# Kernel optimization log

Hardware: AMD Instinct MI355X
Metric: run time of the kernel (lower is better)

## Reference

```python
import jax, jax.numpy as jnp
import numpy as np

L = 4        # num_layers
N = 50000    # nodes
E = 500000   # edges
B = 32       # graphs
H = 64       # hidden_dim
HP = 16      # hidden_dim_pe
P = 8        # pe_dim
BN_EPS = 1e-5


def setup_inputs() -> dict:
    key = jax.random.key(0)
    ks = jax.random.split(key, 22)
    nrm = lambda k, s: jax.random.normal(k, s, dtype=jnp.float32)
    w = lambda k, s: nrm(k, s) * 0.1
    return {
        'x': nrm(ks[0], (N, H)),
        'pe': nrm(ks[1], (N, P)),
        'Lambda': jax.random.uniform(ks[2], (B, P), dtype=jnp.float32),
        'edge_attr': nrm(ks[3], (E, H)),
        'edge_index': jax.random.randint(ks[4], (2, E), 0, N),
        'batch': jnp.sort(jax.random.randint(ks[5], (N,), 0, B)),
        # edge encoder (SPE): eigenvalue MLP + output projection
        'We1': w(ks[6], (L, P, HP * P)), 'be1': jnp.zeros((L, HP * P)),
        'Wee': w(ks[7], (L, HP, H)),     'bee': jnp.zeros((L, H)),
        # GINE mlp: Linear-BN-ReLU-Linear
        'W1': w(ks[8], (L, H, H)), 'b1': jnp.zeros((L, H)),
        'g1': jnp.ones((L, H)),    'beta1': jnp.zeros((L, H)),
        'W2': w(ks[9], (L, H, H)), 'b2': jnp.zeros((L, H)),
        # equivariant PE conv: edge gate + channel Linear
        'Wg': w(ks[10], (L, H, HP)),  'bg': jnp.zeros((L, HP)),
        'Wp': w(ks[11], (L, HP, HP)), 'bp': jnp.zeros((L, HP)),
        # outer BatchNorm per layer
        'gn': jnp.ones((L, H)), 'bnb': jnp.zeros((L, H)),
    }


def _bn(h, gamma, beta):
    mu = h.mean(0)
    var = h.var(0)
    return gamma * (h - mu) * jax.lax.rsqrt(var + BN_EPS) + beta


def reference(x, pe, Lambda, edge_attr, We1, be1, Wee, bee, W1, b1, g1, beta1,
              W2, b2, Wg, bg, Wp, bp, gn, bnb, edge_index, batch):
    src, dst = edge_index[0], edge_index[1]
    bsrc = batch[src]                       # [E] graph id of source node
    z = jnp.tile(pe[:, None, :], (1, HP, 1))  # [N, HP, P]
    for i in range(L):
        # SPE edge encoder: phi(Lambda)-weighted inner product over pe axis
        phi = jax.nn.relu(Lambda @ We1[i] + be1[i]).reshape(B, HP, P)
        eh = jnp.einsum('ehp,ehp->eh', phi[bsrc] * z[src], z[dst])  # [E, HP]
        ea = eh @ Wee[i] + bee[i] + edge_attr                       # [E, H]
        # GINEConv: scatter-add of relu(x_src + edge_attr), eps = 0
        agg = jax.ops.segment_sum(jax.nn.relu(x[src] + ea), dst, num_segments=N)
        h = x + agg
        h = jax.nn.relu(_bn(h @ W1[i] + b1[i], g1[i], beta1[i])) @ W2[i] + b2[i]
        # GINConvEquivariant: gated scatter-add, Linear on channel axis
        gate = jax.nn.relu(ea @ Wg[i] + bg[i])                      # [E, HP]
        msgz = jax.nn.relu(z[src] + gate[:, :, None])               # [E, HP, P]
        z = z + jax.ops.segment_sum(msgz, dst, num_segments=N)
        z = jnp.einsum('nhp,hk->nkp', z, Wp[i]) + bp[i][None, :, None]
        x = _bn(h, gn[i], bnb[i])
        if i != L - 1:
            x = jax.nn.relu(x)
    return x, z
```

## Files before the change

kernel.cpp:

```cpp
#include <hip/hip_runtime.h>

#define NN 50000
#define EE 500000
#define LL 4

typedef unsigned short u16;
typedef unsigned int u32;

__device__ __forceinline__ float bfc(u16 u) { return __uint_as_float(((u32)u) << 16); }
__device__ __forceinline__ u16 f2bf(float f) {
    u32 u = __float_as_uint(f);
    return (u16)((u + 0x7fffu + ((u >> 16) & 1u)) >> 16);
}
__device__ __forceinline__ float lanebc(float v, int l) {
    return __int_as_float(__builtin_amdgcn_readlane(__float_as_int(v), l));
}
__device__ __forceinline__ void unpack2(u32 w, float& lo, float& hi) {
    lo = __uint_as_float(w << 16);
    hi = __uint_as_float(w & 0xffff0000u);
}

__global__ __launch_bounds__(256) void k_init(const float* __restrict__ x, float* __restrict__ Xf,
                                              u16* __restrict__ Xh, int big,
                                              int* __restrict__ deg, int* __restrict__ cursor) {
    for (int i = blockIdx.x * 256 + threadIdx.x; i < NN * 64; i += gridDim.x * 256) {
        if (big) Xh[i] = f2bf(x[i]);
        else Xf[i] = x[i];
    }
    for (int i = blockIdx.x * 256 + threadIdx.x; i < NN; i += gridDim.x * 256) {
        deg[i] = 0;
        cursor[i] = 0;
    }
}

__global__ __launch_bounds__(128) void k_phi(const float* __restrict__ Lam, const float* __restrict__ We1,
                                             const float* __restrict__ be1, float* __restrict__ phiA) {
    int l = blockIdx.x >> 5, b = blockIdx.x & 31, j = threadIdx.x;
    float acc = be1[l * 128 + j];
    for (int q = 0; q < 8; q++)
        acc = fmaf(Lam[b * 8 + q], We1[l * 1024 + q * 128 + j], acc);
    phiA[l * 4096 + b * 128 + j] = fmaxf(acc, 0.f);
}

__global__ __launch_bounds__(256) void k_small(const float* __restrict__ Wee, const float* __restrict__ Wg,
                                               float* __restrict__ MA) {
    int l = blockIdx.x, t = threadIdx.x;
    int k = t >> 4, h = t & 15;
    float m = 0.f;
    for (int f = 0; f < 64; f++)
        m = fmaf(Wee[l * 1024 + k * 64 + f], Wg[l * 1024 + f * 16 + h], m);
    MA[l * 256 + t] = m;
}

__global__ __launch_bounds__(256) void k_hist(const int* __restrict__ ei, int* __restrict__ deg) {
    int e = blockIdx.x * 256 + threadIdx.x;
    if (e < EE) {
        int d = ei[EE + e];
        if (d >= 0 && d < NN) atomicAdd(&deg[d], 1);
    }
}

__global__ __launch_bounds__(256) void k_scan1(const int* __restrict__ deg, int* __restrict__ rowptr,
                                               int* __restrict__ bsum) {
    __shared__ int tmp[256];
    int t = threadIdx.x, i = blockIdx.x * 256 + t;
    int v = (i < NN) ? deg[i] : 0;
    tmp[t] = v;
    __syncthreads();
    for (int off = 1; off < 256; off <<= 1) {
        int a = (t >= off) ? tmp[t - off] : 0;
        __syncthreads();
        tmp[t] += a;
        __syncthreads();
    }
    if (i < NN) rowptr[i] = tmp[t] - v;
    if (t == 255) bsum[blockIdx.x] = tmp[255];
}

__global__ __launch_bounds__(256) void k_scan2(const int* __restrict__ bsum, int* __restrict__ boff,
                                               int* __restrict__ rowptr, int nb) {
    __shared__ int tmp[256];
    int t = threadIdx.x;
    int v = (t < nb) ? bsum[t] : 0;
    tmp[t] = v;
    __syncthreads();
    for (int off = 1; off < 256; off <<= 1) {
        int a = (t >= off) ? tmp[t - off] : 0;
        __syncthreads();
        tmp[t] += a;
        __syncthreads();
    }
    if (t < nb) boff[t] = tmp[t] - v;
    if (t == 255) rowptr[NN] = tmp[255];
}

__global__ __launch_bounds__(256) void k_scan3(int* __restrict__ rowptr, const int* __restrict__ boff) {
    int i = blockIdx.x * 256 + threadIdx.x;
    if (i < NN) rowptr[i] += boff[blockIdx.x];
}

__global__ __launch_bounds__(256) void k_scatter(const int* __restrict__ ei, const int* __restrict__ batch,
                                                 const int* __restrict__ rowptr, int* __restrict__ cursor,
                                                 u32* __restrict__ sb, int* __restrict__ eeo) {
    int e = blockIdx.x * 256 + threadIdx.x;
    if (e < EE) {
        int s = ei[e], d = ei[EE + e];
        if (s < 0) s = 0; if (s >= NN) s = NN - 1;
        if (d < 0) d = 0; if (d >= NN) d = NN - 1;
        int pos = rowptr[d] + atomicAdd(&cursor[d], 1);
        if (pos >= 0 && pos < EE) {
            sb[pos] = (u32)s | ((u32)(batch[s] & 31) << 16);
            eeo[pos] = e;
        }
    }
}

__global__ __launch_bounds__(256) void k_perm(const float* __restrict__ eat, const int* __restrict__ eeo,
                                              u16* __restrict__ eatp) {
    const float4* e4 = reinterpret_cast<const float4*>(eat);
    ushort4* o4 = reinterpret_cast<ushort4*>(eatp);
    for (long long i = (long long)blockIdx.x * 256 + threadIdx.x; i < (long long)EE * 16;
         i += (long long)gridDim.x * 256) {
        int idx = (int)(i >> 4), cc = (int)(i & 15);
        int e = eeo[idx];
        float4 v = e4[(size_t)e * 16 + cc];
        ushort4 o;
        o.x = f2bf(v.x); o.y = f2bf(v.y); o.z = f2bf(v.z); o.w = f2bf(v.w);
        o4[i] = o;
    }
}

__global__ __launch_bounds__(256) void k_eag_all(const u16* __restrict__ eatp, const float* __restrict__ Wg,
                                                 const float* __restrict__ bee, const float* __restrict__ bg,
                                                 u32* __restrict__ EAGp4) {
    __shared__ float sWg[4096];
    __shared__ float scv[64];
    __shared__ u32 srow[256][33];
    const int t = threadIdx.x;
    for (int i = t; i < 4096; i += 256) sWg[i] = Wg[i];
    __syncthreads();
    if (t < 64) {
        const int l = t >> 4, h = t & 15;
        float c = bg[l * 16 + h];
        for (int j = 0; j < 64; j++) c = fmaf(bee[l * 64 + j], sWg[l * 1024 + j * 16 + h], c);
        scv[t] = c;
    }
    const int base = blockIdx.x * 256;
    const u32* eat32 = (const u32*)eatp;
    for (int i = t; i < 256 * 32; i += 256) {
        int r = i >> 5, c = i & 31;
        int idx = base + r;
        srow[r][c] = (idx < EE) ? eat32[(size_t)idx * 32 + c] : 0u;
    }
    __syncthreads();
    const int idx = base + t;
    if (idx >= EE) return;
#pragma unroll
    for (int l = 0; l < LL; l++) {
        const float* wl = &sWg[l * 1024];
        float acc[16];
#pragma unroll
        for (int h = 0; h < 16; h++) acc[h] = scv[l * 16 + h];
#pragma unroll
        for (int c = 0; c < 32; c++) {
            float a0, a1;
            unpack2(srow[t][c], a0, a1);
            const float* w0 = &wl[(2 * c) * 16];
#pragma unroll
            for (int h = 0; h < 16; h++) acc[h] = fmaf(a0, w0[h], fmaf(a1, w0[16 + h], acc[h]));
        }
        u32 w[8];
#pragma unroll
        for (int h = 0; h < 8; h++) w[h] = (u32)f2bf(acc[h]) | ((u32)f2bf(acc[8 + h]) << 16);
        uint4* op = reinterpret_cast<uint4*>(EAGp4 + (size_t)l * EE * 8 + (size_t)idx * 8);
        op[0] = make_uint4(w[0], w[1], w[2], w[3]);
        op[1] = make_uint4(w[4], w[5], w[6], w[7]);
    }
}

__global__ __launch_bounds__(256) void k_eag2(const u16* __restrict__ eatp, const float* __restrict__ WgL,
                                              const float* __restrict__ beeL, const float* __restrict__ bgL,
                                              u32* __restrict__ EAGp) {
    __shared__ float sWg[1024];
    __shared__ float scv[16];
    __shared__ u32 srow[256][33];
    const int t = threadIdx.x;
    for (int i = t; i < 1024; i += 256) sWg[i] = WgL[i];
    __syncthreads();
    if (t < 16) {
        float c = bgL[t];
        for (int j = 0; j < 64; j++) c = fmaf(beeL[j], sWg[j * 16 + t], c);
        scv[t] = c;
    }
    const int base = blockIdx.x * 256;
    const u32* eat32 = (const u32*)eatp;
    for (int i = t; i < 256 * 32; i += 256) {
        int r = i >> 5, c = i & 31;
        int idx = base + r;
        srow[r][c] = (idx < EE) ? eat32[(size_t)idx * 32 + c] : 0u;
    }
    __syncthreads();
    const int idx = base + t;
    if (idx < EE) {
        float acc[16];
#pragma unroll
        for (int h = 0; h < 16; h++) acc[h] = scv[h];
#pragma unroll
        for (int c = 0; c < 32; c++) {
            float a0, a1;
            unpack2(srow[t][c], a0, a1);
            const float* w0 = &sWg[(2 * c) * 16];
#pragma unroll
            for (int h = 0; h < 16; h++) acc[h] = fmaf(a0, w0[h], fmaf(a1, w0[16 + h], acc[h]));
        }
        u32 w[8];
#pragma unroll
        for (int h = 0; h < 8; h++) w[h] = (u32)f2bf(acc[h]) | ((u32)f2bf(acc[8 + h]) << 16);
        uint4* op = reinterpret_cast<uint4*>(EAGp + (size_t)idx * 8);
        op[0] = make_uint4(w[0], w[1], w[2], w[3]);
        op[1] = make_uint4(w[4], w[5], w[6], w[7]);
    }
}

#define EF(P, kk) do { \
    P##w = (u32)__builtin_amdgcn_readlane((int)svec, (kk)); \
    int s_ = (int)(P##w & 0xffffu); \
    if (INM == 0) { P##z0 = P##z1 = pe[s_ * 8 + pp]; } \
    else { float2 t_ = Z2[s_ * 64 + lane]; P##z0 = t_.x; P##z1 = t_.y; } \
    P##xs = bfc(Xh[s_ * 64 + lane]); \
    size_t ge_ = (size_t)(c + (kk)); \
    P##ea = bfc(eatp[ge_ * 64 + lane]); \
    unpack2(EAGp[ge_ * 8 + hlo], P##gl, P##gh); \
} while (0)

#define EC(P, MSK) do { \
    int b_ = (int)((P##w >> 16) & 31u); \
    float p0 = sphi[b_ * 128 + lane] * P##z0 * zd0; \
    float p1 = sphi[b_ * 128 + 64 + lane] * P##z1 * zd1; \
    p0 += __shfl_xor(p0, 1); p1 += __shfl_xor(p1, 1); \
    p0 += __shfl_xor(p0, 2); p1 += __shfl_xor(p1, 2); \
    p0 += __shfl_xor(p0, 4); p1 += __shfl_xor(p1, 4); \
    float eaA = 0.f, eaB = 0.f, gA = P##gl, gB = 0.f, hA = P##gh, hB = 0.f; \
    _Pragma("unroll") \
    for (int k_ = 0; k_ < 8; k_++) { float e_ = lanebc(p0, k_ << 3); \
        eaA = fmaf(e_, wee[k_], eaA); gA = fmaf(e_, mlo[k_], gA); hA = fmaf(e_, mhi[k_], hA); } \
    _Pragma("unroll") \
    for (int k_ = 0; k_ < 8; k_++) { float e_ = lanebc(p1, k_ << 3); \
        eaB = fmaf(e_, wee[8 + k_], eaB); gB = fmaf(e_, mlo[8 + k_], gB); hB = fmaf(e_, mhi[8 + k_], hB); } \
    float ea_ = beev + P##ea + eaA + eaB; \
    accx = fmaf(MSK, fmaxf(0.f, P##xs + ea_), accx); \
    az0  = fmaf(MSK, fmaxf(0.f, P##z0 + fmaxf(gA + gB, 0.f)), az0); \
    az1  = fmaf(MSK, fmaxf(0.f, P##z1 + fmaxf(hA + hB, 0.f)), az1); \
} while (0)

template <int INM, int FIN>
__global__ __launch_bounds__(256) void k_edge2(const float2* __restrict__ Z2,
                                               const float* __restrict__ pe,
                                               const u16* __restrict__ Xh,
                                               const u16* __restrict__ eatp, const u32* __restrict__ EAGp,
                                               const int* __restrict__ rowptr, const u32* __restrict__ sb,
                                               const float* __restrict__ phiL, const float* __restrict__ WeeL,
                                               const float* __restrict__ beeL, const float* __restrict__ ML,
                                               const float* __restrict__ WpL, const float* __restrict__ bpL,
                                               float* __restrict__ Hf, float2* __restrict__ Z2O,
                                               float* __restrict__ outz,
                                               double* __restrict__ stats) {
    __shared__ float sphi[4096];
    __shared__ float sWp[256];
    __shared__ float sbp[16];
    if (blockIdx.x == 0) stats[threadIdx.x] = 0.0;
    for (int t = threadIdx.x; t < 4096; t += 256) sphi[t] = phiL[t];
    if (threadIdx.x < 256) sWp[threadIdx.x] = WpL[threadIdx.x];
    if (threadIdx.x < 16) sbp[threadIdx.x] = bpL[threadIdx.x];
    const int lane = threadIdx.x & 63;
    const int wid = threadIdx.x >> 6;
    const int hlo = lane >> 3;
    const int pp = lane & 7;
    float wee[16], mlo[16], mhi[16];
#pragma unroll
    for (int k = 0; k < 16; k++) {
        wee[k] = WeeL[k * 64 + lane];
        mlo[k] = ML[k * 16 + hlo];
        mhi[k] = ML[k * 16 + 8 + hlo];
    }
    const float beev = beeL[lane];
    __syncthreads();
    for (int n = blockIdx.x * 4 + wid; n < NN; n += gridDim.x * 4) {
        float zd0, zd1;
        if (INM == 0) { zd0 = zd1 = pe[n * 8 + pp]; }
        else { float2 t = Z2[n * 64 + lane]; zd0 = t.x; zd1 = t.y; }
        float accx = bfc(Xh[n * 64 + lane]);
        float az0 = zd0, az1 = zd1;
        int i0 = rowptr[n], i1 = rowptr[n + 1];
        if (i0 < 0) i0 = 0;
        if (i1 > EE) i1 = EE;
        for (int c = i0; c < i1; c += 64) {
            const int ce = (c + 64 < i1) ? c + 64 : i1;
            const int m = ce - c;
            const int mL = m - 1;
            int ci = c + lane; if (ci > i1 - 1) ci = i1 - 1;
            const u32 svec = sb[ci];
            u32 Aw, Bw, Nw, Mw;
            float Az0, Az1, Axs, Aea, Agl, Agh;
            float Bz0, Bz1, Bxs, Bea, Bgl, Bgh;
            float Nz0, Nz1, Nxs, Nea, Ngl, Ngh;
            float Mz0, Mz1, Mxs, Mea, Mgl, Mgh;
            EF(A, 0);
            EF(B, (1 > mL ? mL : 1));
            for (int k = 0; k < m; k += 2) {
                const int n0 = (k + 2 > mL) ? mL : k + 2;
                const int n1 = (k + 3 > mL) ? mL : k + 3;
                EF(N, n0);
                EF(M, n1);
                EC(A, 1.f);
                EC(B, (k + 1 <= mL) ? 1.f : 0.f);
                Aw = Nw; Az0 = Nz0; Az1 = Nz1; Axs = Nxs; Aea = Nea; Agl = Ngl; Agh = Ngh;
                Bw = Mw; Bz0 = Mz0; Bz1 = Mz1; Bxs = Mxs; Bea = Mea; Bgl = Mgl; Bgh = Mgh;
            }
        }
        Hf[n * 64 + lane] = accx;
        float r0 = sbp[hlo], r1 = sbp[8 + hlo];
#pragma unroll
        for (int h = 0; h < 8; h++) {
            const float v = __shfl(az0, (h << 3) + pp);
            r0 = fmaf(v, sWp[h * 16 + hlo], r0);
            r1 = fmaf(v, sWp[h * 16 + 8 + hlo], r1);
        }
#pragma unroll
        for (int h = 0; h < 8; h++) {
            const float v = __shfl(az1, (h << 3) + pp);
            r0 = fmaf(v, sWp[(8 + h) * 16 + hlo], r0);
            r1 = fmaf(v, sWp[(8 + h) * 16 + 8 + hlo], r1);
        }
        if (FIN) {
            outz[n * 128 + lane] = r0;
            outz[n * 128 + 64 + lane] = r1;
        } else {
            Z2O[n * 64 + lane] = make_float2(r0, r1);
        }
    }
}

template <int INM>
__global__ __launch_bounds__(256) void k_edge_s(const float* __restrict__ Zf,
                                                const float* __restrict__ pe,
                                                const float* __restrict__ Xf, const float* __restrict__ eat,
                                                const int* __restrict__ rowptr, const u32* __restrict__ sb,
                                                const int* __restrict__ eeo,
                                                const float* __restrict__ phiL, const float* __restrict__ WeeL,
                                                const float* __restrict__ beeL,
                                                const float* __restrict__ WgL, const float* __restrict__ bgL,
                                                const float* __restrict__ WpL, const float* __restrict__ bpL,
                                                float* __restrict__ Hf, float* __restrict__ ZfO,
                                                double* __restrict__ stats) {
    __shared__ float sphi[32 * 128];
    __shared__ float sWp[256];
    __shared__ float sbp[16];
    if (blockIdx.x == 0) stats[threadIdx.x] = 0.0;
    for (int t = threadIdx.x; t < 4096; t += 256) sphi[t] = phiL[t];
    if (threadIdx.x < 256) sWp[threadIdx.x] = WpL[threadIdx.x];
    if (threadIdx.x < 16) sbp[threadIdx.x] = bpL[threadIdx.x];
    const int lane = threadIdx.x & 63;
    const int wid = threadIdx.x >> 6;
    const int hlo = lane >> 3;
    const int pp = lane & 7;
    const int h16 = lane & 15;
    const int g16 = lane & 48;
    float wee[16], wgr[16];
#pragma unroll
    for (int k = 0; k < 16; k++) {
        wee[k] = WeeL[k * 64 + lane];
        wgr[k] = WgL[(g16 + k) * 16 + h16];
    }
    const float beev = beeL[lane];
    const float bgr = bgL[h16];
    __syncthreads();
    for (int n = blockIdx.x * 4 + wid; n < NN; n += gridDim.x * 4) {
        float zd0, zd1;
        if (INM == 0) { zd0 = zd1 = pe[n * 8 + pp]; }
        else { zd0 = Zf[n * 128 + lane]; zd1 = Zf[n * 128 + 64 + lane]; }
        float accx = Xf[n * 64 + lane];
        float az0 = zd0, az1 = zd1;
        int i0 = rowptr[n], i1 = rowptr[n + 1];
        if (i0 < 0) i0 = 0;
        if (i1 > EE) i1 = EE;
        for (int idx = i0; idx < i1; ++idx) {
            const u32 w = sb[idx];
            const int s = w & 0xffff;
            const int b = (w >> 16) & 31;
            int e = eeo[idx];
            e = (e < 0) ? 0 : ((e >= EE) ? EE - 1 : e);
            float zs0, zs1;
            if (INM == 0) { zs0 = zs1 = pe[s * 8 + pp]; }
            else { zs0 = Zf[s * 128 + lane]; zs1 = Zf[s * 128 + 64 + lane]; }
            float p0 = sphi[b * 128 + lane] * zs0 * zd0;
            float p1 = sphi[b * 128 + 64 + lane] * zs1 * zd1;
            p0 += __shfl_xor(p0, 1); p1 += __shfl_xor(p1, 1);
            p0 += __shfl_xor(p0, 2); p1 += __shfl_xor(p1, 2);
            p0 += __shfl_xor(p0, 4); p1 += __shfl_xor(p1, 4);
            float ea = beev + eat[(size_t)e * 64 + lane];
#pragma unroll
            for (int k = 0; k < 8; k++) ea = fmaf(lanebc(p0, k << 3), wee[k], ea);
#pragma unroll
            for (int k = 0; k < 8; k++) ea = fmaf(lanebc(p1, k << 3), wee[8 + k], ea);
            float gp = 0.f;
#pragma unroll
            for (int i = 0; i < 16; i++) gp = fmaf(__shfl(ea, g16 + i), wgr[i], gp);
            gp += __shfl_xor(gp, 16);
            gp += __shfl_xor(gp, 32);
            const float gv = fmaxf(gp + bgr, 0.f);
            const float glo = __shfl(gv, hlo);
            const float ghi = __shfl(gv, 8 + hlo);
            const float xs = Xf[s * 64 + lane];
            accx += fmaxf(0.f, xs + ea);
            az0 += fmaxf(0.f, zs0 + glo);
            az1 += fmaxf(0.f, zs1 + ghi);
        }
        Hf[n * 64 + lane] = accx;
        float r0 = sbp[hlo], r1 = sbp[8 + hlo];
#pragma unroll
        for (int h = 0; h < 8; h++) {
            const float v = __shfl(az0, (h << 3) + pp);
            r0 = fmaf(v, sWp[h * 16 + hlo], r0);
            r1 = fmaf(v, sWp[h * 16 + 8 + hlo], r1);
        }
#pragma unroll
        for (int h = 0; h < 8; h++) {
            const float v = __shfl(az1, (h << 3) + pp);
            r0 = fmaf(v, sWp[(8 + h) * 16 + hlo], r0);
            r1 = fmaf(v, sWp[(8 + h) * 16 + 8 + hlo], r1);
        }
        ZfO[n * 128 + lane] = r0;
        ZfO[n * 128 + 64 + lane] = r1;
    }
}

__global__ __launch_bounds__(256) void k_gemm1(float* Buf, const float* __restrict__ WL,
                                               const float* __restrict__ bL,
                                               double* __restrict__ sum, double* __restrict__ sq) {
    __shared__ float sW[4096];
    __shared__ double red[512];
    for (int t = threadIdx.x; t < 4096; t += 256) sW[t] = WL[t];
    const int lane = threadIdx.x & 63, wid = threadIdx.x >> 6;
    const float bv = bL[lane];
    __syncthreads();
    double s = 0.0, q = 0.0;
    for (int n = blockIdx.x * 4 + wid; n < NN; n += gridDim.x * 4) {
        const float h = Buf[n * 64 + lane];
        float a0 = bv, a1 = 0.f;
#pragma unroll
        for (int k = 0; k < 32; k++) a0 = fmaf(lanebc(h, k), sW[k * 64 + lane], a0);
#pragma unroll
        for (int k = 32; k < 64; k++) a1 = fmaf(lanebc(h, k), sW[k * 64 + lane], a1);
        const float acc = a0 + a1;
        Buf[n * 64 + lane] = acc;
        s += (double)acc;
        q += (double)acc * (double)acc;
    }
    red[threadIdx.x] = s;
    red[256 + threadIdx.x] = q;
    __syncthreads();
    if (threadIdx.x < 64) {
        s = red[threadIdx.x] + red[threadIdx.x + 64] + red[threadIdx.x + 128] + red[threadIdx.x + 192];
        q = red[256 + threadIdx.x] + red[320 + threadIdx.x] + red[384 + threadIdx.x] + red[448 + threadIdx.x];
        atomicAdd(&sum[lane], s);
        atomicAdd(&sq[lane], q);
    }
}

__global__ __launch_bounds__(256) void k_gemm2(float* Buf, const float* __restrict__ WL,
                                               const float* __restrict__ bL,
                                               const float* __restrict__ gL, const float* __restrict__ betaL,
                                               const double* __restrict__ s1, const double* __restrict__ q1,
                                               double* __restrict__ sum, double* __restrict__ sq) {
    __shared__ float sW[4096];
    __shared__ double red[512];
    for (int t = threadIdx.x; t < 4096; t += 256) sW[t] = WL[t];
    const int lane = threadIdx.x & 63, wid = threadIdx.x >> 6;
    const float bv = bL[lane];
    const double mu = s1[lane] * (1.0 / NN);
    const double var = q1[lane] * (1.0 / NN) - mu * mu;
    const float inv = rsqrtf(fmaxf((float)var, 0.f) + 1e-5f);
    const float gm = gL[lane] * inv;
    const float ga = betaL[lane] - (float)mu * gm;
    __syncthreads();
    double s = 0.0, q = 0.0;
    for (int n = blockIdx.x * 4 + wid; n < NN; n += gridDim.x * 4) {
        const float v = Buf[n * 64 + lane];
        const float r = fmaxf(fmaf(v, gm, ga), 0.f);
        float a0 = bv, a1 = 0.f;
#pragma unroll
        for (int k = 0; k < 32; k++) a0 = fmaf(lanebc(r, k), sW[k * 64 + lane], a0);
#pragma unroll
        for (int k = 32; k < 64; k++) a1 = fmaf(lanebc(r, k), sW[k * 64 + lane], a1);
        const float acc = a0 + a1;
        Buf[n * 64 + lane] = acc;
        s += (double)acc;
        q += (double)acc * (double)acc;
    }
    red[threadIdx.x] = s;
    red[256 + threadIdx.x] = q;
    __syncthreads();
    if (threadIdx.x < 64) {
        s = red[threadIdx.x] + red[threadIdx.x + 64] + red[threadIdx.x + 128] + red[threadIdx.x + 192];
        q = red[256 + threadIdx.x] + red[320 + threadIdx.x] + red[384 + threadIdx.x] + red[448 + threadIdx.x];
        atomicAdd(&sum[lane], s);
        atomicAdd(&sq[lane], q);
    }
}

__global__ __launch_bounds__(256) void k_bnout2(const float* __restrict__ In, u16* __restrict__ Xh,
                                                float* __restrict__ outx,
                                                const double* __restrict__ s2, const double* __restrict__ q2,
                                                const float* __restrict__ gL, const float* __restrict__ bL,
                                                int last) {
    int i = blockIdx.x * 256 + threadIdx.x;
    const int f = i & 63;
    const double mu = s2[f] * (1.0 / NN);
    const double var = q2[f] * (1.0 / NN) - mu * mu;
    const float inv = rsqrtf(fmaxf((float)var, 0.f) + 1e-5f);
    const float gm = gL[f] * inv;
    const float ga = bL[f] - (float)mu * gm;
    for (; i < NN * 64; i += gridDim.x * 256) {
        float o = fmaf(In[i], gm, ga);
        if (last) {
            outx[i] = o;
        } else {
            o = fmaxf(o, 0.f);
            Xh[i] = f2bf(o);
        }
    }
}

__global__ __launch_bounds__(256) void k_bnout(const float* __restrict__ In, float* __restrict__ Xf,
                                               const double* __restrict__ s2, const double* __restrict__ q2,
                                               const float* __restrict__ gL, const float* __restrict__ bL,
                                               int dorelu) {
    int i = blockIdx.x * 256 + threadIdx.x;
    const int f = i & 63;
    const double mu = s2[f] * (1.0 / NN);
    const double var = q2[f] * (1.0 / NN) - mu * mu;
    const float inv = rsqrtf(fmaxf((float)var, 0.f) + 1e-5f);
    const float gm = gL[f] * inv;
    const float ga = bL[f] - (float)mu * gm;
    for (; i < NN * 64; i += gridDim.x * 256) {
        float o = fmaf(In[i], gm, ga);
        if (dorelu) o = fmaxf(o, 0.f);
        Xf[i] = o;
    }
}

extern "C" void kernel_launch(void* const* d_in, const int* in_sizes, int n_in,
                              void* d_out, int out_size, void* d_ws, size_t ws_size,
                              hipStream_t stream) {
    (void)in_sizes; (void)n_in; (void)out_size;
    const float* x    = (const float*)d_in[0];
    const float* pe   = (const float*)d_in[1];
    const float* Lam  = (const float*)d_in[2];
    const float* eat  = (const float*)d_in[3];
    const int*   ei   = (const int*)d_in[4];
    const int*   batch= (const int*)d_in[5];
    const float* We1  = (const float*)d_in[6];
    const float* be1  = (const float*)d_in[7];
    const float* Wee  = (const float*)d_in[8];
    const float* bee  = (const float*)d_in[9];
    const float* W1   = (const float*)d_in[10];
    const float* b1   = (const float*)d_in[11];
    const float* g1   = (const float*)d_in[12];
    const float* bt1  = (const float*)d_in[13];
    const float* W2   = (const float*)d_in[14];
    const float* b2   = (const float*)d_in[15];
    const float* Wg   = (const float*)d_in[16];
    const float* bg   = (const float*)d_in[17];
    const float* Wp   = (const float*)d_in[18];
    const float* bp   = (const float*)d_in[19];
    const float* gn   = (const float*)d_in[20];
    const float* bnb  = (const float*)d_in[21];

    float* Xf   = (float*)d_out;
    u16*   Xh   = (u16*)d_out;
    float* B    = (float*)d_out + 3200000;

    float* A    = (float*)d_ws;
    float* Hf   = A + 6400000;
    float* MA   = Hf + 3200000;
    float* phiA = MA + 1024;
    double* stats = (double*)(phiA + 16384);
    double* s1 = stats, *q1 = stats + 64, *s2 = stats + 128, *q2 = stats + 192;
    int* rowptr = (int*)(stats + 256);
    int* deg    = rowptr + NN + 1;
    int* bsum   = deg + NN;
    int* boff   = bsum + 256;
    int* cursor = boff + 256;
    u32* sb     = (u32*)(cursor + NN);
    int* eeo    = (int*)(sb + EE);
    u16* eatp   = (u16*)(eeo + EE);
    u32* EAGp   = (u32*)(eatp + (size_t)EE * 64);
    const size_t NEED_BIG  = (size_t)((char*)(EAGp + (size_t)EE * 8) - (char*)d_ws);
    const size_t NEED_BIG2 = (size_t)((char*)(EAGp + (size_t)EE * 32) - (char*)d_ws);
    const bool big2 = (ws_size >= NEED_BIG2);
    const bool big  = (ws_size >= NEED_BIG);

    float2* A2 = (float2*)A;
    float2* B2 = (float2*)B;

    const int NB_N = (NN + 255) / 256;
    const int NB_E = (EE + 255) / 256;

    k_init<<<1024, 256, 0, stream>>>(x, Xf, Xh, big ? 1 : 0, deg, cursor);
    k_phi<<<LL * 32, 128, 0, stream>>>(Lam, We1, be1, phiA);
    k_hist<<<NB_E, 256, 0, stream>>>(ei, deg);
    k_scan1<<<NB_N, 256, 0, stream>>>(deg, rowptr, bsum);
    k_scan2<<<1, 256, 0, stream>>>(bsum, boff, rowptr, NB_N);
    k_scan3<<<NB_N, 256, 0, stream>>>(rowptr, boff);
    k_scatter<<<NB_E, 256, 0, stream>>>(ei, batch, rowptr, cursor, sb, eeo);
    if (big) {
        k_small<<<LL, 256, 0, stream>>>(Wee, Wg, MA);
        k_perm<<<4096, 256, 0, stream>>>(eat, eeo, eatp);
        if (big2)
            k_eag_all<<<NB_E, 256, 0, stream>>>(eatp, Wg, bee, bg, EAGp);
    }

    for (int l = 0; l < LL; l++) {
        const float* WeeL = Wee + l * 1024;
        const float* beeL = bee + l * 64;
        const float* WgL  = Wg + l * 1024;
        const float* bgL  = bg + l * 16;
        const float* WpL  = Wp + l * 256;
        const float* bpL  = bp + l * 16;
        const float* phiL = phiA + l * 4096;
        const float* ML   = MA + l * 256;
        if (big) {
            const u32* EAGl = big2 ? (EAGp + (size_t)l * EE * 8) : EAGp;
            if (!big2)
                k_eag2<<<NB_E, 256, 0, stream>>>(eatp, WgL, beeL, bgL, EAGp);
            if (l == 0)
                k_edge2<0, 0><<<6272, 256, 0, stream>>>(A2, pe, Xh, eatp, EAGl, rowptr, sb,
                                                        phiL, WeeL, beeL, ML, WpL, bpL,
                                                        Hf, A2, nullptr, stats);
            else if (l == 1)
                k_edge2<1, 0><<<6272, 256, 0, stream>>>(A2, pe, Xh, eatp, EAGl, rowptr, sb,
                                                        phiL, WeeL, beeL, ML, WpL, bpL,
                                                        Hf, B2, nullptr, stats);
            else if (l == 2)
                k_edge2<1, 0><<<6272, 256, 0, stream>>>(B2, pe, Xh, eatp, EAGl, rowptr, sb,
                                                        phiL, WeeL, beeL, ML, WpL, bpL,
                                                        Hf, A2, nullptr, stats);
            else
                k_edge2<1, 1><<<6272, 256, 0, stream>>>(A2, pe, Xh, eatp, EAGl, rowptr, sb,
                                                        phiL, WeeL, beeL, ML, WpL, bpL,
                                                        Hf, nullptr, B, stats);
        } else {
            const float* Zin  = (l == 2) ? B : A;
            float*       Zout = (l == 1 || l == 3) ? B : A;
            if (l == 0)
                k_edge_s<0><<<2048, 256, 0, stream>>>(nullptr, pe, Xf, eat, rowptr, sb, eeo,
                                                      phiL, WeeL, beeL, WgL, bgL, WpL, bpL,
                                                      Hf, Zout, stats);
            else
                k_edge_s<1><<<2048, 256, 0, stream>>>(Zin, pe, Xf, eat, rowptr, sb, eeo,
                                                      phiL, WeeL, beeL, WgL, bgL, WpL, bpL,
                                                      Hf, Zout, stats);
        }
        k_gemm1<<<512, 256, 0, stream>>>(Hf, W1 + l * 4096, b1 + l * 64, s1, q1);
        k_gemm2<<<512, 256, 0, stream>>>(Hf, W2 + l * 4096, b2 + l * 64,
                                         g1 + l * 64, bt1 + l * 64, s1, q1, s2, q2);
        if (big)
            k_bnout2<<<1024, 256, 0, stream>>>(Hf, Xh, Xf, s2, q2, gn + l * 64, bnb + l * 64,
                                               (l == LL - 1) ? 1 : 0);
        else
            k_bnout<<<1024, 256, 0, stream>>>(Hf, Xf, s2, q2, gn + l * 64, bnb + l * 64,
                                              (l == LL - 1) ? 0 : 1);
    }
}
```

Measured before the change: 1.054 ms.

## Fold outer BatchNorm+ReLU into next layer's edge kernel, drop bnout pass

Removes the separate k_bnout2 pass between layers. k_gemm2 now writes its pre-BN output directly as bf16 into Xh, and the next layer's edge kernel applies the outer BatchNorm affine and ReLU on the fly to each gathered source and destination feature. Per-layer statistics buffers are allocated separately and zeroed once in k_init, so the edge kernel no longer clears them. This saves a full read and write pass over the node features per layer. In exchange the edge gather path does an extra fma and max per load, and the last layer is finalised by a single k_bnout call.

```diff
diff --git a/kernel.cpp b/kernel.cpp
--- a/kernel.cpp
+++ b/kernel.cpp
@@ -22,7 +22,8 @@
 
 __global__ __launch_bounds__(256) void k_init(const float* __restrict__ x, float* __restrict__ Xf,
                                               u16* __restrict__ Xh, int big,
-                                              int* __restrict__ deg, int* __restrict__ cursor) {
+                                              int* __restrict__ deg, int* __restrict__ cursor,
+                                              double* __restrict__ statsAll) {
     for (int i = blockIdx.x * 256 + threadIdx.x; i < NN * 64; i += gridDim.x * 256) {
         if (big) Xh[i] = f2bf(x[i]);
         else Xf[i] = x[i];
@@ -31,6 +32,8 @@
         deg[i] = 0;
         cursor[i] = 0;
     }
+    for (int i = blockIdx.x * 256 + threadIdx.x; i < LL * 256; i += gridDim.x * 256)
+        statsAll[i] = 0.0;
 }
 
 __global__ __launch_bounds__(128) void k_phi(const float* __restrict__ Lam, const float* __restrict__ We1,
@@ -227,7 +230,8 @@
     int s_ = (int)(P##w & 0xffffu); \
     if (INM == 0) { P##z0 = P##z1 = pe[s_ * 8 + pp]; } \
     else { float2 t_ = Z2[s_ * 64 + lane]; P##z0 = t_.x; P##z1 = t_.y; } \
-    P##xs = bfc(Xh[s_ * 64 + lane]); \
+    P##xs = XBN ? fmaxf(0.f, fmaf(bfc(Xh[s_ * 64 + lane]), gmx, gax)) \
+                : bfc(Xh[s_ * 64 + lane]); \
     size_t ge_ = (size_t)(c + (kk)); \
     P##ea = bfc(eatp[ge_ * 64 + lane]); \
     unpack2(EAGp[ge_ * 8 + hlo], P##gl, P##gh); \
@@ -253,7 +257,7 @@
     az1  = fmaf(MSK, fmaxf(0.f, P##z1 + fmaxf(hA + hB, 0.f)), az1); \
 } while (0)
 
-template <int INM, int FIN>
+template <int INM, int FIN, int XBN>
 __global__ __launch_bounds__(256) void k_edge2(const float2* __restrict__ Z2,
                                                const float* __restrict__ pe,
                                                const u16* __restrict__ Xh,
@@ -264,11 +268,11 @@
                                                const float* __restrict__ WpL, const float* __restrict__ bpL,
                                                float* __restrict__ Hf, float2* __restrict__ Z2O,
                                                float* __restrict__ outz,
-                                               double* __restrict__ stats) {
+                                               const float* __restrict__ gnP, const float* __restrict__ bnbP,
+                                               const double* __restrict__ s2P, const double* __restrict__ q2P) {
     __shared__ float sphi[4096];
     __shared__ float sWp[256];
     __shared__ float sbp[16];
-    if (blockIdx.x == 0) stats[threadIdx.x] = 0.0;
     for (int t = threadIdx.x; t < 4096; t += 256) sphi[t] = phiL[t];
     if (threadIdx.x < 256) sWp[threadIdx.x] = WpL[threadIdx.x];
     if (threadIdx.x < 16) sbp[threadIdx.x] = bpL[threadIdx.x];
@@ -284,12 +288,21 @@
         mhi[k] = ML[k * 16 + 8 + hlo];
     }
     const float beev = beeL[lane];
+    float gmx = 1.f, gax = 0.f;
+    if (XBN) {
+        const double mu = s2P[lane] * (1.0 / NN);
+        const double var = q2P[lane] * (1.0 / NN) - mu * mu;
+        const float inv = rsqrtf(fmaxf((float)var, 0.f) + 1e-5f);
+        gmx = gnP[lane] * inv;
+        gax = bnbP[lane] - (float)mu * gmx;
+    }
     __syncthreads();
     for (int n = blockIdx.x * 4 + wid; n < NN; n += gridDim.x * 4) {
         float zd0, zd1;
         if (INM == 0) { zd0 = zd1 = pe[n * 8 + pp]; }
         else { float2 t = Z2[n * 64 + lane]; zd0 = t.x; zd1 = t.y; }
-        float accx = bfc(Xh[n * 64 + lane]);
+        float accx = XBN ? fmaxf(0.f, fmaf(bfc(Xh[n * 64 + lane]), gmx, gax))
+                         : bfc(Xh[n * 64 + lane]);
         float az0 = zd0, az1 = zd1;
         int i0 = rowptr[n], i1 = rowptr[n + 1];
         if (i0 < 0) i0 = 0;
@@ -472,7 +485,8 @@
                                                const float* __restrict__ bL,
                                                const float* __restrict__ gL, const float* __restrict__ betaL,
                                                const double* __restrict__ s1, const double* __restrict__ q1,
-                                               double* __restrict__ sum, double* __restrict__ sq) {
+                                               double* __restrict__ sum, double* __restrict__ sq,
+                                               int out16, u16* __restrict__ XhOut) {
     __shared__ float sW[4096];
     __shared__ double red[512];
     for (int t = threadIdx.x; t < 4096; t += 256) sW[t] = WL[t];
@@ -494,7 +508,8 @@
 #pragma unroll
         for (int k = 32; k < 64; k++) a1 = fmaf(lanebc(r, k), sW[k * 64 + lane], a1);
         const float acc = a0 + a1;
-        Buf[n * 64 + lane] = acc;
+        if (out16) XhOut[n * 64 + lane] = f2bf(acc);
+        else Buf[n * 64 + lane] = acc;
         s += (double)acc;
         q += (double)acc * (double)acc;
     }
@@ -506,29 +521,6 @@
         q = red[256 + threadIdx.x] + red[320 + threadIdx.x] + red[384 + threadIdx.x] + red[448 + threadIdx.x];
         atomicAdd(&sum[lane], s);
         atomicAdd(&sq[lane], q);
-    }
-}
-
-__global__ __launch_bounds__(256) void k_bnout2(const float* __restrict__ In, u16* __restrict__ Xh,
-                                                float* __restrict__ outx,
-                                                const double* __restrict__ s2, const double* __restrict__ q2,
-                                                const float* __restrict__ gL, const float* __restrict__ bL,
-                                                int last) {
-    int i = blockIdx.x * 256 + threadIdx.x;
-    const int f = i & 63;
-    const double mu = s2[f] * (1.0 / NN);
-    const double var = q2[f] * (1.0 / NN) - mu * mu;
-    const float inv = rsqrtf(fmaxf((float)var, 0.f) + 1e-5f);
-    const float gm = gL[f] * inv;
-    const float ga = bL[f] - (float)mu * gm;
-    for (; i < NN * 64; i += gridDim.x * 256) {
-        float o = fmaf(In[i], gm, ga);
-        if (last) {
-            outx[i] = o;
-        } else {
-            o = fmaxf(o, 0.f);
-            Xh[i] = f2bf(o);
-        }
     }
 }
 
@@ -586,8 +578,7 @@
     float* MA   = Hf + 3200000;
     float* phiA = MA + 1024;
     double* stats = (double*)(phiA + 16384);
-    double* s1 = stats, *q1 = stats + 64, *s2 = stats + 128, *q2 = stats + 192;
-    int* rowptr = (int*)(stats + 256);
+    int* rowptr = (int*)(stats + LL * 256);
     int* deg    = rowptr + NN + 1;
     int* bsum   = deg + NN;
     int* boff   = bsum + 256;
@@ -607,7 +598,7 @@
     const int NB_N = (NN + 255) / 256;
     const int NB_E = (EE + 255) / 256;
 
-    k_init<<<1024, 256, 0, stream>>>(x, Xf, Xh, big ? 1 : 0, deg, cursor);
+    k_init<<<1024, 256, 0, stream>>>(x, Xf, Xh, big ? 1 : 0, deg, cursor, stats);
     k_phi<<<LL * 32, 128, 0, stream>>>(Lam, We1, be1, phiA);
     k_hist<<<NB_E, 256, 0, stream>>>(ei, deg);
     k_scan1<<<NB_N, 256, 0, stream>>>(deg, rowptr, bsum);
@@ -630,46 +621,63 @@
         const float* bpL  = bp + l * 16;
         const float* phiL = phiA + l * 4096;
         const float* ML   = MA + l * 256;
+        double* sl = stats + l * 256;
         if (big) {
             const u32* EAGl = big2 ? (EAGp + (size_t)l * EE * 8) : EAGp;
             if (!big2)
                 k_eag2<<<NB_E, 256, 0, stream>>>(eatp, WgL, beeL, bgL, EAGp);
+            const double* s2p = stats + (l - 1) * 256 + 128;
+            const double* q2p = stats + (l - 1) * 256 + 192;
+            const float* gnp  = gn + (l - 1) * 64;
+            const float* bnbp = bnb + (l - 1) * 64;
             if (l == 0)
-                k_edge2<0, 0><<<6272, 256, 0, stream>>>(A2, pe, Xh, eatp, EAGl, rowptr, sb,
-                                                        phiL, WeeL, beeL, ML, WpL, bpL,
-                                                        Hf, A2, nullptr, stats);
+                k_edge2<0, 0, 0><<<6272, 256, 0, stream>>>(A2, pe, Xh, eatp, EAGl, rowptr, sb,
+                                                           phiL, WeeL, beeL, ML, WpL, bpL,
+                                                           Hf, A2, nullptr,
+                                                           nullptr, nullptr, nullptr, nullptr);
             else if (l == 1)
-                k_edge2<1, 0><<<6272, 256, 0, stream>>>(A2, pe, Xh, eatp, EAGl, rowptr, sb,
-                                                        phiL, WeeL, beeL, ML, WpL, bpL,
-                                                        Hf, B2, nullptr, stats);
+                k_edge2<1, 0, 1><<<6272, 256, 0, stream>>>(A2, pe, Xh, eatp, EAGl, rowptr, sb,
+                                                           phiL, WeeL, beeL, ML, WpL, bpL,
+                                                           Hf, B2, nullptr,
+                                                           gnp, bnbp, s2p, q2p);
             else if (l == 2)
-                k_edge2<1, 0><<<6272, 256, 0, stream>>>(B2, pe, Xh, eatp, EAGl, rowptr, sb,
-                                                        phiL, WeeL, beeL, ML, WpL, bpL,
-                                                        Hf, A2, nullptr, stats);
+                k_edge2<1, 0, 1><<<6272, 256, 0, stream>>>(B2, pe, Xh, eatp, EAGl, rowptr, sb,
+                                                           phiL, WeeL, beeL, ML, WpL, bpL,
+                                                           Hf, A2, nullptr,
+                                                           gnp, bnbp, s2p, q2p);
             else
-                k_edge2<1, 1><<<6272, 256, 0, stream>>>(A2, pe, Xh, eatp, EAGl, rowptr, sb,
-                                                        phiL, WeeL, beeL, ML, WpL, bpL,
-                                                        Hf, nullptr, B, stats);
+                k_edge2<1, 1, 1><<<6272, 256, 0, stream>>>(A2, pe, Xh, eatp, EAGl, rowptr, sb,
+                                                           phiL, WeeL, beeL, ML, WpL, bpL,
+                                                           Hf, nullptr, B,
+                                                           gnp, bnbp, s2p, q2p);
+            k_gemm1<<<512, 256, 0, stream>>>(Hf, W1 + l * 4096, b1 + l * 64, sl, sl + 64);
+            k_gemm2<<<512, 256, 0, stream>>>(Hf, W2 + l * 4096, b2 + l * 64,
+                                             g1 + l * 64, bt1 + l * 64, sl, sl + 64,
+                                             sl + 128, sl + 192,
+                                             (l < LL - 1) ? 1 : 0, Xh);
         } else {
             const float* Zin  = (l == 2) ? B : A;
             float*       Zout = (l == 1 || l == 3) ? B : A;
             if (l == 0)
                 k_edge_s<0><<<2048, 256, 0, stream>>>(nullptr, pe, Xf, eat, rowptr, sb, eeo,
                                                       phiL, WeeL, beeL, WgL, bgL, WpL, bpL,
-                                                      Hf, Zout, stats);
+                                                      Hf, Zout, sl);
             else
                 k_edge_s<1><<<2048, 256, 0, stream>>>(Zin, pe, Xf, eat, rowptr, sb, eeo,
                                                       phiL, WeeL, beeL, WgL, bgL, WpL, bpL,
-                                                      Hf, Zout, stats);
-        }
-        k_gemm1<<<512, 256, 0, stream>>>(Hf, W1 + l * 4096, b1 + l * 64, s1, q1);
-        k_gemm2<<<512, 256, 0, stream>>>(Hf, W2 + l * 4096, b2 + l * 64,
-                                         g1 + l * 64, bt1 + l * 64, s1, q1, s2, q2);
-        if (big)
-            k_bnout2<<<1024, 256, 0, stream>>>(Hf, Xh, Xf, s2, q2, gn + l * 64, bnb + l * 64,
-                                               (l == LL - 1) ? 1 : 0);
-        else
-            k_bnout<<<1024, 256, 0, stream>>>(Hf, Xf, s2, q2, gn + l * 64, bnb + l * 64,
+                                                      Hf, Zout, sl);
+            k_gemm1<<<512, 256, 0, stream>>>(Hf, W1 + l * 4096, b1 + l * 64, sl, sl + 64);
+            k_gemm2<<<512, 256, 0, stream>>>(Hf, W2 + l * 4096, b2 + l * 64,
+                                             g1 + l * 64, bt1 + l * 64, sl, sl + 64,
+                                             sl + 128, sl + 192, 0, nullptr);
+            k_bnout<<<1024, 256, 0, stream>>>(Hf, Xf, sl + 128, sl + 192,
+                                              gn + l * 64, bnb + l * 64,
                                               (l == LL - 1) ? 0 : 1);
-    }
-}
+        }
+    }
+    if (big) {
+        double* sl3 = stats + (LL - 1) * 256;
+        k_bnout<<<1024, 256, 0, stream>>>(Hf, Xf, sl3 + 128, sl3 + 192,
+                                          gn + (LL - 1) * 64, bnb + (LL - 1) * 64, 0);
+    }
+}
```

Result: faster. 1.004 ms, median of 2 (-4.8%).
